# Performance work log

Hardware: AMD Instinct MI355X
Metric: run time of the kernel (lower is better)

## Reference

```python
import jax, jax.numpy as jnp
import numpy as np

# bitsandbytes NF4 codebook (16 levels)
NF4_CODE = jnp.array([
    -1.0, -0.6961928009986877, -0.5250730514526367, -0.39491748809814453,
    -0.28444138169288635, -0.18477343022823334, -0.09105003625154495, 0.0,
    0.07958029955625534, 0.16093020141124725, 0.24611230194568634,
    0.33791524171829224, 0.44070982933044434, 0.5626170039176941,
    0.7229568362236023, 1.0], dtype=jnp.float32)

L, D, KV, F, V = 2, 4096, 1024, 14336, 32000   # layers, d_model, kv_dim, ffn, vocab
H, HK, HD = 32, 8, 128                          # q heads, kv heads, head dim
B, S = 2, 1024
BLK = 64                                        # NF4 quant blocksize
ROPE_THETA = 500000.0
RMS_EPS = 1e-5


def _dequant(idx, absmax, shape):
    # idx: uint8 flat codes in [0,16); absmax: fp32 per-64-element block scale
    w = NF4_CODE[idx.astype(jnp.int32)]
    return (w.reshape(-1, BLK) * absmax[:, None]).reshape(shape)


def _rmsnorm(x, w):
    return x * jax.lax.rsqrt(jnp.mean(x * x, axis=-1, keepdims=True) + RMS_EPS) * w


def _rope(x, cos, sin):
    d2 = x.shape[-1] // 2
    x1, x2 = x[..., :d2], x[..., d2:]
    return jnp.concatenate([x1 * cos - x2 * sin, x2 * cos + x1 * sin], axis=-1)


def setup_inputs() -> dict:
    key = jax.random.key(0)
    ks = iter(jax.random.split(key, 64))

    def idx(n):
        return jax.random.randint(next(ks), (n,), 0, 16).astype(jnp.uint8)

    def amax(n):
        return jax.random.uniform(next(ks), (n // BLK,), minval=0.01, maxval=0.05)

    def qw(n):
        return (jnp.stack([idx(n) for _ in range(L)]),
                jnp.stack([amax(n) for _ in range(L)]))

    inp = {}
    inp["input_ids"] = jax.random.randint(next(ks), (B, S), 0, V, dtype=jnp.int32)
    inp["attention_mask"] = jnp.ones((B, S), dtype=jnp.int32)
    inp["embed"] = jax.random.normal(next(ks), (V, D), dtype=jnp.float32) * 0.02
    inp["q_idx"], inp["q_absmax"] = qw(D * D)
    inp["k_idx"], inp["k_absmax"] = qw(KV * D)
    inp["v_idx"], inp["v_absmax"] = qw(KV * D)
    inp["o_idx"], inp["o_absmax"] = qw(D * D)
    inp["gate_idx"], inp["gate_absmax"] = qw(F * D)
    inp["up_idx"], inp["up_absmax"] = qw(F * D)
    inp["down_idx"], inp["down_absmax"] = qw(D * F)
    inp["ln1_w"] = jnp.ones((L, D), dtype=jnp.float32)
    inp["ln2_w"] = jnp.ones((L, D), dtype=jnp.float32)
    inp["final_ln_w"] = jnp.ones((D,), dtype=jnp.float32)
    return inp


def reference(input_ids, attention_mask, embed,
              q_idx, q_absmax, k_idx, k_absmax, v_idx, v_absmax,
              o_idx, o_absmax, gate_idx, gate_absmax, up_idx, up_absmax,
              down_idx, down_absmax, ln1_w, ln2_w, final_ln_w):
    b, s = input_ids.shape
    h = embed[input_ids]                                  # [B,S,D]
    pos = jnp.arange(s, dtype=jnp.float32)
    inv = 1.0 / (ROPE_THETA ** (jnp.arange(0, HD, 2, dtype=jnp.float32) / HD))
    ang = pos[:, None] * inv[None, :]                     # [S,HD/2]
    cos = jnp.cos(ang)[None, :, None, :]
    sin = jnp.sin(ang)[None, :, None, :]
    causal = jnp.tril(jnp.ones((s, s), dtype=bool))
    mask = causal[None, None] & (attention_mask[:, None, None, :] > 0)  # [B,1,S,S]
    neg = jnp.finfo(h.dtype).min

    for l in range(L):
        x = _rmsnorm(h, ln1_w[l])
        q = x @ _dequant(q_idx[l], q_absmax[l], (D, D)).T
        k = x @ _dequant(k_idx[l], k_absmax[l], (KV, D)).T
        v = x @ _dequant(v_idx[l], v_absmax[l], (KV, D)).T
        q = _rope(q.reshape(b, s, H, HD), cos, sin)
        k = _rope(k.reshape(b, s, HK, HD), cos, sin)
        v = v.reshape(b, s, HK, HD)
        k = jnp.repeat(k, H // HK, axis=2)                # GQA expand
        v = jnp.repeat(v, H // HK, axis=2)
        scores = jnp.einsum('bqhd,bkhd->bhqk', q, k) / np.float32(np.sqrt(HD))
        scores = jnp.where(mask, scores, neg)
        attn = jax.nn.softmax(scores, axis=-1)
        ctx = jnp.einsum('bhqk,bkhd->bqhd', attn, v).reshape(b, s, D)
        h = h + ctx @ _dequant(o_idx[l], o_absmax[l], (D, D)).T
        x = _rmsnorm(h, ln2_w[l])
        g = x @ _dequant(gate_idx[l], gate_absmax[l], (F, D)).T
        u = x @ _dequant(up_idx[l], up_absmax[l], (F, D)).T
        h = h + (jax.nn.silu(g) * u) @ _dequant(down_idx[l], down_absmax[l], (D, F)).T

    h = _rmsnorm(h, final_ln_w)                           # last hidden state
    m = attention_mask.astype(h.dtype)[..., None]         # masked mean pool
    pooled = (h * m).sum(axis=1) / jnp.clip(m.sum(axis=1), 1e-9)
    return pooled
```

## Files before the change

kernel.cpp:

```cpp
#include <hip/hip_runtime.h>
#include <hip/hip_fp16.h>
#include <cstdint>
#include <cstddef>

#define B_  2
#define S_  1024
#define D_  4096
#define KV_ 1024
#define F_  14336
#define H_  32
#define HK_ 8
#define HD_ 128
#define M_  2048

typedef _Float16 f16;
typedef f16   f16x8 __attribute__((ext_vector_type(8)));
typedef f16   f16x4 __attribute__((ext_vector_type(4)));
typedef float f32x4 __attribute__((ext_vector_type(4)));

#define AS1(p) ((const __attribute__((address_space(1))) void*)(p))
#define AS3(p) ((__attribute__((address_space(3))) void*)(p))

__device__ __constant__ float NF4_C[16] = {
 -1.0f, -0.6961928009986877f, -0.5250730514526367f, -0.39491748809814453f,
 -0.28444138169288635f, -0.18477343022823334f, -0.09105003625154495f, 0.0f,
 0.07958029955625534f, 0.16093020141124725f, 0.24611230194568634f,
 0.33791524171829224f, 0.44070982933044434f, 0.5626170039176941f,
 0.7229568362236023f, 1.0f };

__global__ void k_detect(const unsigned* __restrict__ p, int* __restrict__ flag){
    if (threadIdx.x == 0){
        int u8 = 0;
        for (int i = 0; i < 256; ++i) if (p[i] >= 16u) { u8 = 1; break; }
        *flag = u8;
    }
}

__global__ __launch_bounds__(256) void k_dequant(const void* __restrict__ idxBase, size_t elemOff,
        const float* __restrict__ amax, f16* __restrict__ out, const int* __restrict__ flag)
{
    __shared__ __half2 T[3856];
    int t = threadIdx.x;
    if (t < 256){
        int b0 = t & 15, b1 = t >> 4;
        T[b0 + (b1 << 8)] = __halves2half2(__float2half(NF4_C[b0]), __float2half(NF4_C[b1]));
    }
    __syncthreads();
    size_t i = ((size_t)blockIdx.x * 256 + t) * 16;
    float am = amax[i >> 6];
    __half2 am2 = __float2half2_rn(am);
    union { __half2 h2[8]; uint4 u4[2]; } R;
    if (*flag){
        uint4 u = *(const uint4*)((const uint8_t*)idxBase + elemOff + i);
        unsigned w[4] = {u.x, u.y, u.z, u.w};
        #pragma unroll
        for (int j = 0; j < 4; ++j){
            R.h2[j*2+0] = __hmul2(T[w[j] & 0xFFFFu], am2);
            R.h2[j*2+1] = __hmul2(T[w[j] >> 16],     am2);
        }
    } else {
        const int4* s4 = (const int4*)((const int*)idxBase + elemOff + i);
        #pragma unroll
        for (int j = 0; j < 4; ++j){
            int4 a = s4[j];
            R.h2[j*2+0] = __hmul2(T[a.x | (a.y << 8)], am2);
            R.h2[j*2+1] = __hmul2(T[a.z | (a.w << 8)], am2);
        }
    }
    uint4* o = (uint4*)(out + i);
    o[0] = R.u4[0]; o[1] = R.u4[1];
}

__global__ __launch_bounds__(256) void k_embed(const int* __restrict__ ids,
        const float* __restrict__ E, float* __restrict__ Hh)
{
    int row = blockIdx.x, t = threadIdx.x;
    int id = ids[row];
    const float4* s4 = (const float4*)(E + (size_t)id * D_);
    float4* d4 = (float4*)(Hh + (size_t)row * D_);
    #pragma unroll
    for (int i = 0; i < 4; ++i) d4[t + 256*i] = s4[t + 256*i];
}

__global__ __launch_bounds__(256) void k_ropetab(float* __restrict__ cosT, float* __restrict__ sinT){
    int id = blockIdx.x * 256 + threadIdx.x;
    int d = id & 63, s = id >> 6;
    float inv = powf(500000.0f, -(float)d * (1.0f/64.0f));
    float ang = (float)s * inv;
    cosT[id] = cosf(ang);
    sinT[id] = sinf(ang);
}

template<int F16OUT>
__global__ __launch_bounds__(256) void k_rmsnorm(const float* __restrict__ X,
        const float* __restrict__ W, void* __restrict__ outv)
{
    int row = blockIdx.x, t = threadIdx.x;
    const float4* x4 = (const float4*)(X + (size_t)row * D_);
    float4 xs[4]; float ss = 0.f;
    #pragma unroll
    for (int i = 0; i < 4; ++i){
        xs[i] = x4[t + 256*i];
        ss += xs[i].x*xs[i].x + xs[i].y*xs[i].y + xs[i].z*xs[i].z + xs[i].w*xs[i].w;
    }
    for (int m = 32; m; m >>= 1) ss += __shfl_xor(ss, m, 64);
    __shared__ float red[4];
    if ((t & 63) == 0) red[t >> 6] = ss;
    __syncthreads();
    ss = red[0] + red[1] + red[2] + red[3];
    float rs = rsqrtf(ss * (1.0f / D_) + 1e-5f);
    #pragma unroll
    for (int i = 0; i < 4; ++i){
        int c0 = (t + 256*i) * 4;
        float4 wv = *(const float4*)(W + c0);
        float o0 = xs[i].x*rs*wv.x, o1 = xs[i].y*rs*wv.y;
        float o2 = xs[i].z*rs*wv.z, o3 = xs[i].w*rs*wv.w;
        if (F16OUT){
            f16x4 ov = { (f16)o0, (f16)o1, (f16)o2, (f16)o3 };
            *(f16x4*)((f16*)outv + (size_t)row * D_ + c0) = ov;
        } else {
            float4 ov = {o0, o1, o2, o3};
            *(float4*)((float*)outv + (size_t)row * D_ + c0) = ov;
        }
    }
}

template<int LNH>
__global__ __launch_bounds__(256) void k_rope(const f16* __restrict__ in, int istr,
        f16* __restrict__ outp, const float* __restrict__ cosT, const float* __restrict__ sinT)
{
    int p = blockIdx.x * 256 + threadIdx.x;
    int d = p & 63;
    int h = (p >> 6) & ((1 << LNH) - 1);
    int s = (p >> (6 + LNH)) & (S_ - 1);
    int b = p >> (16 + LNH);
    size_t ib = (size_t)(b * S_ + s) * istr + (size_t)h * HD_;
    float x1 = (float)in[ib + d], x2 = (float)in[ib + 64 + d];
    float c = cosT[s*64 + d], sn = sinT[s*64 + d];
    size_t ob = (((size_t)((b << LNH) + h)) * S_ + (size_t)s) * HD_;
    outp[ob + d]      = (f16)(x1 * c - x2 * sn);
    outp[ob + 64 + d] = (f16)(x2 * c + x1 * sn);
}

__global__ __launch_bounds__(256) void k_vtrans(const f16* __restrict__ in, int istr,
        f16* __restrict__ outp){
    int p = blockIdx.x * 256 + threadIdx.x;
    int s  = p & (S_ - 1);
    int d  = (p >> 10) & (HD_ - 1);
    int hk = (p >> 17) & (HK_ - 1);
    int b  = p >> 20;
    f16 v = in[(size_t)(b * S_ + s) * istr + (size_t)hk * HD_ + d];
    outp[(((size_t)(b * HK_ + hk)) * HD_ + d) * S_ + s] = v;
}

__global__ __launch_bounds__(256) void k_softmax(__half* __restrict__ P, const int* __restrict__ amask, int bh0){
    int rid = blockIdx.x;
    int z = rid >> 10, sq = rid & (S_ - 1);
    int b = (bh0 + z) >> 5;
    __half* row = P + (size_t)z * S_ * S_ + (size_t)sq * S_;
    int t = threadIdx.x;
    const __half2* r2 = (const __half2*)row;
    __half2 a0 = r2[t*2], a1 = r2[t*2 + 1];
    float v[4] = { __low2float(a0), __high2float(a0), __low2float(a1), __high2float(a1) };
    int c0 = t * 4;
    #pragma unroll
    for (int j = 0; j < 4; ++j){
        int col = c0 + j;
        if (col > sq || amask[b * S_ + col] == 0) v[j] = -1e30f;
    }
    float mx = fmaxf(fmaxf(v[0], v[1]), fmaxf(v[2], v[3]));
    for (int m = 32; m; m >>= 1) mx = fmaxf(mx, __shfl_xor(mx, m, 64));
    __shared__ float red[4];
    if ((t & 63) == 0) red[t >> 6] = mx;
    __syncthreads();
    mx = fmaxf(fmaxf(red[0], red[1]), fmaxf(red[2], red[3]));
    float p4[4], sum = 0.f;
    #pragma unroll
    for (int j = 0; j < 4; ++j){ p4[j] = __expf(v[j] - mx); sum += p4[j]; }
    for (int m = 32; m; m >>= 1) sum += __shfl_xor(sum, m, 64);
    __syncthreads();
    if ((t & 63) == 0) red[t >> 6] = sum;
    __syncthreads();
    sum = red[0] + red[1] + red[2] + red[3];
    float inv = 1.0f / fmaxf(sum, 1e-30f);
    __half2* w2 = (__half2*)row;
    w2[t*2]     = __floats2half2_rn(p4[0]*inv, p4[1]*inv);
    w2[t*2 + 1] = __floats2half2_rn(p4[2]*inv, p4[3]*inv);
}

template<int OUT, int BM>
__global__ __launch_bounds__(256) void k_gemm(const f16* __restrict__ A, const f16* __restrict__ Bp,
        void* __restrict__ Cv, const f16* __restrict__ G,
        int Kd, int ldc, float scale, int bh0)
{
    __shared__ f16 As[128 * 64];
    __shared__ f16 Bs[128 * 64];
    int t = threadIdx.x;
    int wave = t >> 6, lane = t & 63;
    int wr = wave >> 1, wc = wave & 1;
    int lr = lane & 15, lg = lane >> 4;
    int row0 = blockIdx.y * 128, col0 = blockIdx.x * 128;

    size_t aOff = 0, bOff = 0, cOff = 0;
    if (BM == 1){
        if (col0 > row0 + 127) return;
        int bh = bh0 + blockIdx.z;
        aOff = (size_t)bh * (S_ * HD_);
        bOff = (size_t)((bh >> 5) * HK_ + ((bh & 31) >> 2)) * (S_ * HD_);
        cOff = (size_t)blockIdx.z * (S_ * S_);
    } else if (BM == 2){
        int bh = bh0 + blockIdx.z;
        aOff = (size_t)blockIdx.z * (S_ * S_);
        bOff = (size_t)((bh >> 5) * HK_ + ((bh & 31) >> 2)) * (HD_ * S_);
        cOff = (size_t)(bh >> 5) * ((size_t)S_ * D_) + (size_t)(bh & 31) * HD_;
        Kd = row0 + 128;
    }

    f32x4 zero = {0.f, 0.f, 0.f, 0.f};
    f32x4 acc[4][4];
    #pragma unroll
    for (int m = 0; m < 4; ++m)
        #pragma unroll
        for (int n = 0; n < 4; ++n) acc[m][n] = zero;

    int srow = lane >> 3;
    int scol = (lane & 7) * 8;
    const f16* Abase = A  + aOff + (size_t)row0 * Kd;
    const f16* Bbase = Bp + bOff + (size_t)col0 * Kd;
    if (BM == 1){ Abase = A + aOff + (size_t)row0 * Kd; Bbase = Bp + bOff + (size_t)col0 * Kd; }
    if (BM == 2){ Abase = A + aOff + (size_t)row0 * S_; Bbase = Bp + bOff + (size_t)col0 * S_; }

    int lda = (BM == 2) ? S_ : Kd;
    for (int k0 = 0; k0 < Kd; k0 += 64){
        if (k0) __syncthreads();
        #pragma unroll
        for (int i = 0; i < 4; ++i){
            int chunk = wave * 4 + i;
            int r = chunk * 8 + srow;
            __builtin_amdgcn_global_load_lds(AS1(Abase + (size_t)r * lda + k0 + scol), AS3(&As[chunk * 512]), 16, 0, 0);
            __builtin_amdgcn_global_load_lds(AS1(Bbase + (size_t)r * lda + k0 + scol), AS3(&Bs[chunk * 512]), 16, 0, 0);
        }
        __syncthreads();
        #pragma unroll
        for (int kk = 0; kk < 64; kk += 32){
            f16x8 av[4], bv[4];
            #pragma unroll
            for (int m = 0; m < 4; ++m) av[m] = *(const f16x8*)&As[(wr*64 + m*16 + lr)*64 + kk + lg*8];
            #pragma unroll
            for (int n = 0; n < 4; ++n) bv[n] = *(const f16x8*)&Bs[(wc*64 + n*16 + lr)*64 + kk + lg*8];
            #pragma unroll
            for (int m = 0; m < 4; ++m)
                #pragma unroll
                for (int n = 0; n < 4; ++n)
                    acc[m][n] = __builtin_amdgcn_mfma_f32_16x16x32_f16(av[m], bv[n], acc[m][n], 0, 0, 0);
        }
    }

    #pragma unroll
    for (int m = 0; m < 4; ++m)
    #pragma unroll
    for (int n = 0; n < 4; ++n)
    #pragma unroll
    for (int r = 0; r < 4; ++r){
        int row = row0 + wr*64 + m*16 + lg*4 + r;
        int col = col0 + wc*64 + n*16 + lr;
        size_t idx = cOff + (size_t)row * ldc + col;
        float v = acc[m][n][r] * scale;
        ((f16*)Cv)[idx] = (f16)v;
    }
}

template<int OUT>
__global__ __launch_bounds__(512, 1) void k_gemm3(const f16* __restrict__ A, const f16* __restrict__ Bp,
        void* __restrict__ Cv, const f16* __restrict__ G, int Kd, int ldk, int ldc)
{
    __shared__ f16 LDS[65536];
    const int t = threadIdx.x;
    const int w = t >> 6, l = t & 63;
    const int wm = w >> 2, wn = w & 3;

    int gx = gridDim.x, gy = gridDim.y;
    int nWG = gx * gy * gridDim.z;
    int n = (blockIdx.z * gy + blockIdx.y) * gx + blockIdx.x;
    int q = nWG >> 3;
    int sw = (n & 7) * q + (n >> 3);
    int bx = sw % gx; int r1 = sw / gx; int by = r1 % gy; int bz = r1 / gy;

    const int row0 = by * 256, col0 = bx * 256;
    const size_t koff = (size_t)bz * Kd;
    const int NT = Kd >> 6;

    const int swzk = ((t & 7) ^ ((t >> 3) & 7)) * 8;
    const f16* pA[2]; const f16* pB[2];
    #pragma unroll
    for (int l2 = 0; l2 < 2; ++l2){
        pA[l2] = A  + (size_t)(row0 + l2*128 + (t >> 3)) * ldk + koff + swzk;
        int wnc = (l2*64 + (t >> 3)) >> 5;
        pB[l2] = Bp + (size_t)(col0 + wnc*64 + ((t >> 3) & 31)) * ldk + koff + swzk;
    }

    auto stA = [&](int g, int tt, int buf){
        size_t so = (size_t)tt * 64;
        #pragma unroll
        for (int l2 = 0; l2 < 2; ++l2)
            __builtin_amdgcn_global_load_lds(AS1(pA[l2] + (size_t)g*64*ldk + so),
                AS3(&LDS[buf*16384 + g*8192 + l2*4096 + w*512]), 16, 0, 0);
    };
    auto stB = [&](int g, int tt, int buf){
        size_t so = (size_t)tt * 64;
        #pragma unroll
        for (int l2 = 0; l2 < 2; ++l2)
            __builtin_amdgcn_global_load_lds(AS1(pB[l2] + (size_t)g*32*ldk + so),
                AS3(&LDS[32768 + buf*16384 + g*8192 + l2*4096 + w*512]), 16, 0, 0);
    };

    const int lrow = (l & 15) * 64;
    const int kp0 = (((l >> 4))     ^ (l & 7)) * 8;
    const int kp1 = ((4 + (l >> 4)) ^ (l & 7)) * 8;

    f16x8 aR[2][4], bR0[2][2], bR1[2][2];
    auto rdA = [&](int g, int buf){
        int base = buf*16384 + g*8192 + wm*4096 + lrow;
        #pragma unroll
        for (int mf = 0; mf < 4; ++mf){
            aR[0][mf] = *(const f16x8*)&LDS[base + mf*1024 + kp0];
            aR[1][mf] = *(const f16x8*)&LDS[base + mf*1024 + kp1];
        }
    };
    auto rdB = [&](int g, int buf, f16x8 (&bR)[2][2]){
        int base = 32768 + buf*16384 + g*8192 + wn*2048 + lrow;
        #pragma unroll
        for (int nf = 0; nf < 2; ++nf){
            bR[0][nf] = *(const f16x8*)&LDS[base + nf*1024 + kp0];
            bR[1][nf] = *(const f16x8*)&LDS[base + nf*1024 + kp1];
        }
    };

    f32x4 zero = {0.f, 0.f, 0.f, 0.f};
    f32x4 acc[8][4];
    #pragma unroll
    for (int mi = 0; mi < 8; ++mi)
        #pragma unroll
        for (int ni = 0; ni < 4; ++ni) acc[mi][ni] = zero;

    #define MMQ(qm, qn, bR) { \
        __builtin_amdgcn_s_setprio(1); \
        _Pragma("unroll") \
        for (int ks = 0; ks < 2; ++ks) \
            _Pragma("unroll") \
            for (int mf = 0; mf < 4; ++mf) \
                _Pragma("unroll") \
                for (int nf = 0; nf < 2; ++nf) \
                    acc[(qm)*4+mf][(qn)*2+nf] = __builtin_amdgcn_mfma_f32_16x16x32_f16(aR[ks][mf], bR[ks][nf], acc[(qm)*4+mf][(qn)*2+nf], 0, 0, 0); \
        __builtin_amdgcn_s_setprio(0); }
    #define LGKM0 { asm volatile("s_waitcnt lgkmcnt(0)" ::: "memory"); __builtin_amdgcn_sched_barrier(0); }
    #define VM4   { asm volatile("s_waitcnt vmcnt(4)" ::: "memory"); }
    #define BAR   __builtin_amdgcn_s_barrier()

    stA(0, 0, 0); stB(1, 0, 0); stA(1, 0, 0); stB(0, 0, 0);
    if (NT > 1){ stA(0, 1, 1); stB(1, 1, 1); }
    VM4; BAR;

    for (int tt = 0; tt < NT; tt += 2){
        int c2 = (tt + 2 < NT) ? tt + 2 : NT - 1;
        int c3 = (tt + 3 < NT) ? tt + 3 : NT - 1;
        rdA(0, 0); rdB(0, 0, bR0);
        stA(1, tt+1 < NT ? tt+1 : NT-1, 1); stB(0, tt+1 < NT ? tt+1 : NT-1, 1);
        BAR; LGKM0; MMQ(0, 0, bR0); BAR;
        rdB(1, 0, bR1);
        BAR; LGKM0; MMQ(0, 1, bR1); BAR;
        rdA(1, 0);
        stA(0, c2, 0);
        BAR; LGKM0; MMQ(1, 1, bR1); BAR;
        stB(1, c2, 0);
        BAR; MMQ(1, 0, bR0); VM4; BAR;
        rdA(0, 1); rdB(0, 1, bR0);
        stA(1, c2, 0); stB(0, c2, 0);
        BAR; LGKM0; MMQ(0, 0, bR0); BAR;
        rdB(1, 1, bR1);
        BAR; LGKM0; MMQ(0, 1, bR1); BAR;
        rdA(1, 1);
        stA(0, c3, 1);
        BAR; LGKM0; MMQ(1, 1, bR1); BAR;
        stB(1, c3, 1);
        BAR; MMQ(1, 0, bR0); VM4; BAR;
    }

    #pragma unroll
    for (int mi = 0; mi < 8; ++mi)
    #pragma unroll
    for (int ni = 0; ni < 4; ++ni)
    #pragma unroll
    for (int r = 0; r < 4; ++r){
        int row = row0 + wm*128 + mi*16 + ((l >> 4) << 2) + r;
        int col = col0 + wn*64  + ni*16 + (l & 15);
        float v = acc[mi][ni][r];
        if (OUT == 0){
            ((float*)Cv)[(size_t)bz * ((size_t)M_ * ldc) + (size_t)row * ldc + col] = v;
        } else if (OUT == 2){
            ((f16*)Cv)[(size_t)row * ldc + col] = (f16)v;
        } else {
            size_t idx = (size_t)row * ldc + col;
            float g = (float)G[idx];
            float sg = g / (1.f + __expf(-g));
            ((f16*)Cv)[idx] = (f16)(sg * v);
        }
    }
    #undef MMQ
    #undef LGKM0
    #undef VM4
    #undef BAR
}

__global__ __launch_bounds__(256) void k_comb(const float* __restrict__ p0, const float* __restrict__ p1,
        float* __restrict__ outv)
{
    size_t i = ((size_t)blockIdx.x * 256 + threadIdx.x) * 4;
    float4 a = *(const float4*)(p0 + i);
    float4 b = *(const float4*)(p1 + i);
    float4 hv = *(const float4*)(outv + i);
    hv.x += a.x + b.x; hv.y += a.y + b.y; hv.z += a.z + b.z; hv.w += a.w + b.w;
    *(float4*)(outv + i) = hv;
}

__global__ __launch_bounds__(256) void k_pool1(const float* __restrict__ Hn, const int* __restrict__ amask,
        float* __restrict__ part, float* __restrict__ cntp)
{
    int d0 = blockIdx.x * 256 + threadIdx.x;
    int b  = blockIdx.y;
    int z  = blockIdx.z;
    int s0 = z * 128;
    float s = 0.f;
    for (int i = 0; i < 128; ++i){
        int row = s0 + i;
        if (amask[b * S_ + row])
            s += Hn[((size_t)(b * S_ + row)) * D_ + d0];
    }
    part[((size_t)(z * B_ + b)) * D_ + d0] = s;
    if (blockIdx.x == 0 && threadIdx.x == 0){
        float c = 0.f;
        for (int i = 0; i < 128; ++i) c += (amask[b * S_ + s0 + i] != 0) ? 1.f : 0.f;
        cntp[z * B_ + b] = c;
    }
}
__global__ __launch_bounds__(256) void k_pool2(const float* __restrict__ part, const float* __restrict__ cntp,
        float* __restrict__ outp)
{
    int gid = blockIdx.x * 256 + threadIdx.x;
    int b = gid >> 12, d = gid & (D_ - 1);
    float s = 0.f, c = 0.f;
    #pragma unroll
    for (int z = 0; z < 8; ++z){
        s += part[((size_t)(z * B_ + b)) * D_ + d];
        c += cntp[z * B_ + b];
    }
    outp[gid] = s / fmaxf(c, 1e-9f);
}

extern "C" void kernel_launch(void* const* d_in, const int* in_sizes, int n_in,
                              void* d_out, int out_size, void* d_ws, size_t ws_size,
                              hipStream_t stream)
{
    (void)in_sizes; (void)n_in; (void)out_size; (void)ws_size;
    const int*   ids   = (const int*)  d_in[0];
    const int*   amask = (const int*)  d_in[1];
    const float* embed = (const float*)d_in[2];
    const void*  qi = d_in[3];  const float* qa = (const float*)d_in[4];
    const void*  ki = d_in[5];  const float* ka = (const float*)d_in[6];
    const void*  vi = d_in[7];  const float* va = (const float*)d_in[8];
    const void*  oi = d_in[9];  const float* oa = (const float*)d_in[10];
    const void*  gi = d_in[11]; const float* ga = (const float*)d_in[12];
    const void*  ui = d_in[13]; const float* ua = (const float*)d_in[14];
    const void*  di = d_in[15]; const float* da = (const float*)d_in[16];
    const float* ln1 = (const float*)d_in[17];
    const float* ln2 = (const float*)d_in[18];
    const float* lnf = (const float*)d_in[19];

    const size_t DD  = (size_t)D_ * D_;
    const size_t KVD = (size_t)KV_ * D_;
    const size_t FD  = (size_t)F_ * D_;

    char* ws = (char*)d_ws;
    int*   flag = (int*)ws;
    float* h    = (float*)(ws + 256);
    float* cosT = (float*)(ws + 256 + 33554432);
    float* sinT = cosT + 65536;
    f16*   xin  = (f16*)(ws + 34078976);
    f16*   wbuf = (f16*)(ws + 50856192);
    char*  R4   = ws + 168296704;
    f16* qkv16 = (f16*)(R4);
    f16* qr  = (f16*)(R4 + 25165824);
    f16* kr  = (f16*)(R4 + 41943040);
    f16* vtr = (f16*)(R4 + 46137344);
    f16* ctx = (f16*)(R4 + 50331648);
    char* R5 = R4 + 67108864;
    __half* scores = (__half*)R5;
    f16*    gbuf   = (f16*)R5;
    float*  pR5_0  = (float*)R5;
    float*  pR5_1  = (float*)(R5 + 33554432);
    float*  pR4_0  = (float*)R4;
    float*  pR4_1  = (float*)(R4 + 33554432);
    float*  hn     = (float*)R4;
    float*  part   = (float*)R5;
    float*  cntp   = (float*)(R5 + 1048576);

    const float ISQ = 0.08838834764831845f;
    const int QKV_N = D_ + 2 * KV_;

    k_detect <<<1, 64, 0, stream>>>((const unsigned*)qi, flag);
    k_embed  <<<M_, 256, 0, stream>>>(ids, embed, h);
    k_ropetab<<<256, 256, 0, stream>>>(cosT, sinT);

    for (int l = 0; l < 2; ++l){
        size_t oDD = (size_t)l * DD, oKVD = (size_t)l * KVD, oFD = (size_t)l * FD;
        k_rmsnorm<1><<<M_, 256, 0, stream>>>(h, ln1 + l * D_, xin);

        k_dequant<<<DD / 4096, 256, 0, stream>>>(qi, oDD, qa + oDD/64, wbuf, flag);
        k_dequant<<<KVD / 4096, 256, 0, stream>>>(ki, oKVD, ka + oKVD/64, wbuf + DD, flag);
        k_dequant<<<KVD / 4096, 256, 0, stream>>>(vi, oKVD, va + oKVD/64, wbuf + DD + KVD, flag);
        k_gemm3<2><<<dim3(QKV_N/256, M_/256, 1), 512, 0, stream>>>(xin, wbuf, qkv16, nullptr, D_, D_, QKV_N);

        k_rope<5><<<(B_*S_*H_*64)/256, 256, 0, stream>>>(qkv16, QKV_N, qr, cosT, sinT);
        k_rope<3><<<(B_*S_*HK_*64)/256, 256, 0, stream>>>(qkv16 + D_, QKV_N, kr, cosT, sinT);
        k_vtrans <<<(B_*HK_*HD_*S_)/256, 256, 0, stream>>>(qkv16 + D_ + KV_, QKV_N, vtr);

        for (int c = 0; c < 2; ++c){
            k_gemm<2,1><<<dim3(S_/128, S_/128, 32), 256, 0, stream>>>(qr, kr, (void*)scores, nullptr, HD_, S_, ISQ, c*32);
            k_softmax<<<32 * S_, 256, 0, stream>>>(scores, amask, c*32);
            k_gemm<2,2><<<dim3(1, S_/128, 32), 256, 0, stream>>>((const f16*)scores, vtr, ctx, nullptr, S_, D_, 1.0f, c*32);
        }

        k_dequant<<<DD / 4096, 256, 0, stream>>>(oi, oDD, oa + oDD/64, wbuf, flag);
        k_gemm3<0><<<dim3(D_/256, M_/256, 2), 512, 0, stream>>>(ctx, wbuf, pR5_0, nullptr, D_/2, D_, D_);
        k_comb<<<(M_*D_)/1024, 256, 0, stream>>>(pR5_0, pR5_1, h);

        k_rmsnorm<1><<<M_, 256, 0, stream>>>(h, ln2 + l * D_, xin);
        k_dequant<<<FD / 4096, 256, 0, stream>>>(gi, oFD, ga + oFD/64, wbuf, flag);
        k_gemm3<2><<<dim3(F_/256, M_/256, 1), 512, 0, stream>>>(xin, wbuf, gbuf, nullptr, D_, D_, F_);
        k_dequant<<<FD / 4096, 256, 0, stream>>>(ui, oFD, ua + oFD/64, wbuf, flag);
        k_gemm3<3><<<dim3(F_/256, M_/256, 1), 512, 0, stream>>>(xin, wbuf, gbuf, gbuf, D_, D_, F_);
        k_dequant<<<FD / 4096, 256, 0, stream>>>(di, oFD, da + oFD/64, wbuf, flag);
        k_gemm3<0><<<dim3(D_/256, M_/256, 2), 512, 0, stream>>>(gbuf, wbuf, pR4_0, nullptr, F_/2, F_, D_);
        k_comb<<<(M_*D_)/1024, 256, 0, stream>>>(pR4_0, pR4_1, h);
    }

    k_rmsnorm<0><<<M_, 256, 0, stream>>>(h, lnf, hn);
    k_pool1<<<dim3(D_/256, B_, 8), 256, 0, stream>>>(hn, amask, part, cntp);
    k_pool2<<<(B_*D_)/256, 256, 0, stream>>>(part, cntp, (float*)d_out);
}
```

Before: 2.663 ms.

## Switch main GEMM to 32x32 MFMA tiles and batch attention over all heads

The main NF4 GEMM kernel moves from 16x16x32 MFMA fragments to 32x32x16 MFMA instructions with f32x16 accumulators. The LDS read pattern and epilogue index mapping are rewritten to match. This cuts the instruction count and LDS reads per FLOP. Separately, the attention path now runs all 64 batch-heads in one launch each for scores, softmax and PV instead of two chunks of 32. That needs a larger scores buffer at a new workspace offset, which risks overrunning the workspace if it is not large enough.

```diff
diff --git a/kernel.cpp b/kernel.cpp
--- a/kernel.cpp
+++ b/kernel.cpp
@@ -17,6 +17,7 @@
 typedef f16   f16x8 __attribute__((ext_vector_type(8)));
 typedef f16   f16x4 __attribute__((ext_vector_type(4)));
 typedef float f32x4 __attribute__((ext_vector_type(4)));
+typedef float f32x16 __attribute__((ext_vector_type(16)));
 
 #define AS1(p) ((const __attribute__((address_space(1))) void*)(p))
 #define AS3(p) ((__attribute__((address_space(3))) void*)(p))
@@ -153,10 +154,10 @@
     outp[(((size_t)(b * HK_ + hk)) * HD_ + d) * S_ + s] = v;
 }
 
-__global__ __launch_bounds__(256) void k_softmax(__half* __restrict__ P, const int* __restrict__ amask, int bh0){
+__global__ __launch_bounds__(256) void k_softmax(__half* __restrict__ P, const int* __restrict__ amask){
     int rid = blockIdx.x;
     int z = rid >> 10, sq = rid & (S_ - 1);
-    int b = (bh0 + z) >> 5;
+    int b = z >> 5;
     __half* row = P + (size_t)z * S_ * S_ + (size_t)sq * S_;
     int t = threadIdx.x;
     const __half2* r2 = (const __half2*)row;
@@ -225,10 +226,10 @@
 
     int srow = lane >> 3;
     int scol = (lane & 7) * 8;
-    const f16* Abase = A  + aOff + (size_t)row0 * Kd;
-    const f16* Bbase = Bp + bOff + (size_t)col0 * Kd;
-    if (BM == 1){ Abase = A + aOff + (size_t)row0 * Kd; Bbase = Bp + bOff + (size_t)col0 * Kd; }
+    const f16* Abase;
+    const f16* Bbase;
     if (BM == 2){ Abase = A + aOff + (size_t)row0 * S_; Bbase = Bp + bOff + (size_t)col0 * S_; }
+    else        { Abase = A + aOff + (size_t)row0 * Kd; Bbase = Bp + bOff + (size_t)col0 * Kd; }
 
     int lda = (BM == 2) ? S_ : Kd;
     for (int k0 = 0; k0 < Kd; k0 += 64){
@@ -278,6 +279,7 @@
     const int t = threadIdx.x;
     const int w = t >> 6, l = t & 63;
     const int wm = w >> 2, wn = w & 3;
+    const int l5 = l >> 5, l31 = l & 31, lx = l & 7;
 
     int gx = gridDim.x, gy = gridDim.y;
     int nWG = gx * gy * gridDim.z;
@@ -314,44 +316,37 @@
                 AS3(&LDS[32768 + buf*16384 + g*8192 + l2*4096 + w*512]), 16, 0, 0);
     };
 
-    const int lrow = (l & 15) * 64;
-    const int kp0 = (((l >> 4))     ^ (l & 7)) * 8;
-    const int kp1 = ((4 + (l >> 4)) ^ (l & 7)) * 8;
-
-    f16x8 aR[2][4], bR0[2][2], bR1[2][2];
-    auto rdA = [&](int g, int buf){
-        int base = buf*16384 + g*8192 + wm*4096 + lrow;
-        #pragma unroll
-        for (int mf = 0; mf < 4; ++mf){
-            aR[0][mf] = *(const f16x8*)&LDS[base + mf*1024 + kp0];
-            aR[1][mf] = *(const f16x8*)&LDS[base + mf*1024 + kp1];
-        }
+    f16x8 aF[2][4], bF0[4], bF1[4];
+    auto rdA32 = [&](int qm, int buf){
+        int base = buf*16384 + qm*8192 + wm*4096 + l31*64;
+        #pragma unroll
+        for (int mi = 0; mi < 2; ++mi)
+            #pragma unroll
+            for (int kst = 0; kst < 4; ++kst)
+                aF[mi][kst] = *(const f16x8*)&LDS[base + mi*2048 + (((kst*2 + l5) ^ lx) << 3)];
     };
-    auto rdB = [&](int g, int buf, f16x8 (&bR)[2][2]){
-        int base = 32768 + buf*16384 + g*8192 + wn*2048 + lrow;
-        #pragma unroll
-        for (int nf = 0; nf < 2; ++nf){
-            bR[0][nf] = *(const f16x8*)&LDS[base + nf*1024 + kp0];
-            bR[1][nf] = *(const f16x8*)&LDS[base + nf*1024 + kp1];
-        }
+    auto rdB32 = [&](int qn, int buf, f16x8 (&bF)[4]){
+        int base = 32768 + buf*16384 + qn*8192 + wn*2048 + l31*64;
+        #pragma unroll
+        for (int kst = 0; kst < 4; ++kst)
+            bF[kst] = *(const f16x8*)&LDS[base + (((kst*2 + l5) ^ lx) << 3)];
     };
 
-    f32x4 zero = {0.f, 0.f, 0.f, 0.f};
-    f32x4 acc[8][4];
-    #pragma unroll
-    for (int mi = 0; mi < 8; ++mi)
-        #pragma unroll
-        for (int ni = 0; ni < 4; ++ni) acc[mi][ni] = zero;
-
-    #define MMQ(qm, qn, bR) { \
+    f32x16 acc[4][2];
+    #pragma unroll
+    for (int mt = 0; mt < 4; ++mt)
+        #pragma unroll
+        for (int nt = 0; nt < 2; ++nt)
+            #pragma unroll
+            for (int r = 0; r < 16; ++r) acc[mt][nt][r] = 0.f;
+
+    #define MMQ32(qm, qn, bF) { \
         __builtin_amdgcn_s_setprio(1); \
         _Pragma("unroll") \
-        for (int ks = 0; ks < 2; ++ks) \
+        for (int kst = 0; kst < 4; ++kst) \
             _Pragma("unroll") \
-            for (int mf = 0; mf < 4; ++mf) \
-                _Pragma("unroll") \
-                for (int nf = 0; nf < 2; ++nf) \
-                    acc[(qm)*4+mf][(qn)*2+nf] = __builtin_amdgcn_mfma_f32_16x16x32_f16(aR[ks][mf], bR[ks][nf], acc[(qm)*4+mf][(qn)*2+nf], 0, 0, 0); \
+            for (int mi = 0; mi < 2; ++mi) \
+                acc[(qm)*2+mi][qn] = __builtin_amdgcn_mfma_f32_32x32x16_f16(aF[mi][kst], bF[kst], acc[(qm)*2+mi][qn], 0, 0, 0); \
         __builtin_amdgcn_s_setprio(0); }
     #define LGKM0 { asm volatile("s_waitcnt lgkmcnt(0)" ::: "memory"); __builtin_amdgcn_sched_barrier(0); }
     #define VM4   { asm volatile("s_waitcnt vmcnt(4)" ::: "memory"); }
@@ -364,37 +359,37 @@
     for (int tt = 0; tt < NT; tt += 2){
         int c2 = (tt + 2 < NT) ? tt + 2 : NT - 1;
         int c3 = (tt + 3 < NT) ? tt + 3 : NT - 1;
-        rdA(0, 0); rdB(0, 0, bR0);
+        rdA32(0, 0); rdB32(0, 0, bF0);
         stA(1, tt+1 < NT ? tt+1 : NT-1, 1); stB(0, tt+1 < NT ? tt+1 : NT-1, 1);
-        BAR; LGKM0; MMQ(0, 0, bR0); BAR;
-        rdB(1, 0, bR1);
-        BAR; LGKM0; MMQ(0, 1, bR1); BAR;
-        rdA(1, 0);
+        BAR; LGKM0; MMQ32(0, 0, bF0); BAR;
+        rdB32(1, 0, bF1);
+        BAR; LGKM0; MMQ32(0, 1, bF1); BAR;
+        rdA32(1, 0);
         stA(0, c2, 0);
-        BAR; LGKM0; MMQ(1, 1, bR1); BAR;
+        BAR; LGKM0; MMQ32(1, 1, bF1); BAR;
         stB(1, c2, 0);
-        BAR; MMQ(1, 0, bR0); VM4; BAR;
-        rdA(0, 1); rdB(0, 1, bR0);
+        BAR; MMQ32(1, 0, bF0); VM4; BAR;
+        rdA32(0, 1); rdB32(0, 1, bF0);
         stA(1, c2, 0); stB(0, c2, 0);
-        BAR; LGKM0; MMQ(0, 0, bR0); BAR;
-        rdB(1, 1, bR1);
-        BAR; LGKM0; MMQ(0, 1, bR1); BAR;
-        rdA(1, 1);
+        BAR; LGKM0; MMQ32(0, 0, bF0); BAR;
+        rdB32(1, 1, bF1);
+        BAR; LGKM0; MMQ32(0, 1, bF1); BAR;
+        rdA32(1, 1);
         stA(0, c3, 1);
-        BAR; LGKM0; MMQ(1, 1, bR1); BAR;
+        BAR; LGKM0; MMQ32(1, 1, bF1); BAR;
         stB(1, c3, 1);
-        BAR; MMQ(1, 0, bR0); VM4; BAR;
-    }
-
-    #pragma unroll
-    for (int mi = 0; mi < 8; ++mi)
-    #pragma unroll
-    for (int ni = 0; ni < 4; ++ni)
-    #pragma unroll
-    for (int r = 0; r < 4; ++r){
-        int row = row0 + wm*128 + mi*16 + ((l >> 4) << 2) + r;
-        int col = col0 + wn*64  + ni*16 + (l & 15);
-        float v = acc[mi][ni][r];
+        BAR; MMQ32(1, 0, bF0); VM4; BAR;
+    }
+
+    #pragma unroll
+    for (int mt = 0; mt < 4; ++mt)
+    #pragma unroll
+    for (int nt = 0; nt < 2; ++nt)
+    #pragma unroll
+    for (int rg = 0; rg < 16; ++rg){
+        int row = row0 + wm*128 + mt*32 + (rg & 3) + ((rg >> 2) << 3) + (l5 << 2);
+        int col = col0 + wn*64 + nt*32 + l31;
+        float v = acc[mt][nt][rg];
         if (OUT == 0){
             ((float*)Cv)[(size_t)bz * ((size_t)M_ * ldc) + (size_t)row * ldc + col] = v;
         } else if (OUT == 2){
@@ -406,7 +401,7 @@
             ((f16*)Cv)[idx] = (f16)(sg * v);
         }
     }
-    #undef MMQ
+    #undef MMQ32
     #undef LGKM0
     #undef VM4
     #undef BAR
@@ -494,7 +489,6 @@
     f16* vtr = (f16*)(R4 + 46137344);
     f16* ctx = (f16*)(R4 + 50331648);
     char* R5 = R4 + 67108864;
-    __half* scores = (__half*)R5;
     f16*    gbuf   = (f16*)R5;
     float*  pR5_0  = (float*)R5;
     float*  pR5_1  = (float*)(R5 + 33554432);
@@ -503,6 +497,7 @@
     float*  hn     = (float*)R4;
     float*  part   = (float*)R5;
     float*  cntp   = (float*)(R5 + 1048576);
+    __half* scores = (__half*)(ws + 310378496);
 
     const float ISQ = 0.08838834764831845f;
     const int QKV_N = D_ + 2 * KV_;
@@ -524,11 +519,9 @@
         k_rope<3><<<(B_*S_*HK_*64)/256, 256, 0, stream>>>(qkv16 + D_, QKV_N, kr, cosT, sinT);
         k_vtrans <<<(B_*HK_*HD_*S_)/256, 256, 0, stream>>>(qkv16 + D_ + KV_, QKV_N, vtr);
 
-        for (int c = 0; c < 2; ++c){
-            k_gemm<2,1><<<dim3(S_/128, S_/128, 32), 256, 0, stream>>>(qr, kr, (void*)scores, nullptr, HD_, S_, ISQ, c*32);
-            k_softmax<<<32 * S_, 256, 0, stream>>>(scores, amask, c*32);
-            k_gemm<2,2><<<dim3(1, S_/128, 32), 256, 0, stream>>>((const f16*)scores, vtr, ctx, nullptr, S_, D_, 1.0f, c*32);
-        }
+        k_gemm<2,1><<<dim3(S_/128, S_/128, 64), 256, 0, stream>>>(qr, kr, (void*)scores, nullptr, HD_, S_, ISQ, 0);
+        k_softmax<<<64 * S_, 256, 0, stream>>>(scores, amask);
+        k_gemm<2,2><<<dim3(1, S_/128, 64), 256, 0, stream>>>((const f16*)scores, vtr, ctx, nullptr, S_, D_, 1.0f, 0);
 
         k_dequant<<<DD / 4096, 256, 0, stream>>>(oi, oDD, oa + oDD/64, wbuf, flag);
         k_gemm3<0><<<dim3(D_/256, M_/256, 2), 512, 0, stream>>>(ctx, wbuf, pR5_0, nullptr, D_/2, D_, D_);
```

Result: slower. 2.881 ms (+8.2%).
